# Kernel tuning notes

Measured on AMD Instinct MI355X. Metric: run time of the kernel, lower is better.

## Reference

```python
import jax, jax.numpy as jnp
import numpy as np

IMG_H, IMG_W = 800, 1216
NUM_CLASSES = 91
NUM_ANCHORS = 9
C_FPN = 256
LEVEL_HW = [(100, 152), (50, 76), (25, 38), (13, 19), (7, 10)]
SCORE_T = 0.05
NMS_T = 0.5
TOPK = 1000
MAX_DET = 300
BBOX_CLIP = float(np.log(1000.0 / 16.0))
NEG = -1e9


def make_anchors():
    # torchvision AnchorGenerator: sizes (x, x*2^(1/3), x*2^(2/3)) for x in [32..512], ratios (0.5,1,2)
    sizes = [(32, 40, 50), (64, 80, 101), (128, 161, 203), (256, 322, 406), (512, 645, 812)]
    ratios = np.array([0.5, 1.0, 2.0], dtype=np.float64)
    levels = []
    for (H, W), sc in zip(LEVEL_HW, sizes):
        scales = np.array(sc, dtype=np.float64)
        h_r = np.sqrt(ratios)
        w_r = 1.0 / h_r
        ws = (w_r[:, None] * scales[None, :]).reshape(-1)
        hs = (h_r[:, None] * scales[None, :]).reshape(-1)
        base = np.round(np.stack([-ws, -hs, ws, hs], axis=1) / 2.0)  # [9,4]
        sx = IMG_W // W
        sy = IMG_H // H
        shift_x = np.arange(W, dtype=np.float64) * sx
        shift_y = np.arange(H, dtype=np.float64) * sy
        yy, xx = np.meshgrid(shift_y, shift_x, indexing='ij')
        shifts = np.stack([xx, yy, xx, yy], axis=-1).reshape(-1, 1, 4)  # [HW,1,4]
        levels.append((shifts + base[None]).reshape(-1, 4).astype(np.float32))  # [HW*9,4]
    return levels


def _conv(x, w, b):
    y = jax.lax.conv_general_dilated(x, w, (1, 1), 'SAME', dimension_numbers=('NCHW', 'OIHW', 'NCHW'))
    return y + b[None, :, None, None]


def _gn(x, g, b, groups=32, eps=1e-5):
    N, C, H, W = x.shape
    xr = x.reshape(N, groups, C // groups, H, W)
    mu = xr.mean((2, 3, 4), keepdims=True)
    var = xr.var((2, 3, 4), keepdims=True)
    xr = (xr - mu) * jax.lax.rsqrt(var + eps)
    return xr.reshape(N, C, H, W) * g[None, :, None, None] + b[None, :, None, None]


def _tower(x, tw, tb, gs, gb):
    for i in range(4):  # fixed 4-layer conv tower
        x = jax.nn.relu(_gn(_conv(x, tw[i], tb[i]), gs[i], gb[i]))
    return x


def _decode(rel, anc):
    # torchvision BoxCoder decode, weights (1,1,1,1)
    w = anc[:, 2] - anc[:, 0]
    h = anc[:, 3] - anc[:, 1]
    cx = anc[:, 0] + 0.5 * w
    cy = anc[:, 1] + 0.5 * h
    dx, dy = rel[:, 0], rel[:, 1]
    dw = jnp.minimum(rel[:, 2], BBOX_CLIP)
    dh = jnp.minimum(rel[:, 3], BBOX_CLIP)
    pcx = dx * w + cx
    pcy = dy * h + cy
    pw = jnp.exp(dw) * w
    ph = jnp.exp(dh) * h
    return jnp.stack([pcx - 0.5 * pw, pcy - 0.5 * ph, pcx + 0.5 * pw, pcy + 0.5 * ph], axis=-1)


def _iou_one(box, boxes):
    lt = jnp.maximum(box[:2], boxes[:, :2])
    rb = jnp.minimum(box[2:], boxes[:, 2:])
    wh = jnp.clip(rb - lt, 0.0)
    inter = wh[:, 0] * wh[:, 1]
    a1 = (box[2] - box[0]) * (box[3] - box[1])
    a2 = (boxes[:, 2] - boxes[:, 0]) * (boxes[:, 3] - boxes[:, 1])
    return inter / (a1 + a2 - inter + 1e-9)


def _nms(boxes, scores, labels):
    # class-aware NMS via per-class coordinate offset, fixed MAX_DET iterations
    off = labels.astype(boxes.dtype) * float(IMG_W + IMG_H + 1)
    b_off = boxes + off[:, None]

    def body(ws, _):
        j = jnp.argmax(ws)
        s = ws[j]
        sup = _iou_one(b_off[j], b_off) > NMS_T
        ws = jnp.where(sup, NEG, ws)
        ws = ws.at[j].set(NEG)
        return ws, (j, s)

    _, (idxs, svals) = jax.lax.scan(body, scores, None, length=MAX_DET)
    valid = svals > 0.0
    out_boxes = jnp.where(valid[:, None], boxes[idxs], 0.0)
    out_scores = jnp.where(valid, svals, 0.0)
    out_labels = jnp.where(valid, labels[idxs], -1)
    return out_boxes, out_scores, out_labels


def _post_one(cls_l, reg_l, anc_l):
    bxs, scs, lbs = [], [], []
    for cl, rg, an in zip(cls_l, reg_l, anc_l):
        s = jax.nn.sigmoid(cl).reshape(-1)  # [HW*9*91]
        s = jnp.where(s > SCORE_T, s, -1.0)
        v, i = jax.lax.top_k(s, TOPK)
        ai = i // NUM_CLASSES
        lb = i % NUM_CLASSES
        bxs.append(_decode(rg[ai], an[ai]))
        scs.append(v)
        lbs.append(lb)
    boxes = jnp.concatenate(bxs)
    scores = jnp.concatenate(scs)
    labels = jnp.concatenate(lbs).astype(jnp.int32)
    boxes = jnp.stack([jnp.clip(boxes[:, 0], 0, IMG_W), jnp.clip(boxes[:, 1], 0, IMG_H),
                       jnp.clip(boxes[:, 2], 0, IMG_W), jnp.clip(boxes[:, 3], 0, IMG_H)], axis=-1)
    scores = jnp.where(scores > SCORE_T, scores, NEG)
    return _nms(boxes, scores, labels)


def setup_inputs() -> dict:
    key = jax.random.key(0)
    ks = jax.random.split(key, 16)
    d = {}
    for n, (name, (H, W)) in enumerate(zip(['p3', 'p4', 'p5', 'p6', 'p7'], LEVEL_HW)):
        d[name] = jax.random.normal(ks[n], (2, C_FPN, H, W), jnp.float32)
    std = 0.01
    d['cls_tw'] = jax.random.normal(ks[5], (4, C_FPN, C_FPN, 3, 3), jnp.float32) * std
    d['cls_tb'] = jnp.zeros((4, C_FPN), jnp.float32)
    d['cls_gs'] = jnp.ones((4, C_FPN), jnp.float32)
    d['cls_gb'] = jnp.zeros((4, C_FPN), jnp.float32)
    d['cls_w'] = jax.random.normal(ks[6], (NUM_ANCHORS * NUM_CLASSES, C_FPN, 3, 3), jnp.float32) * std
    d['cls_b'] = jnp.full((NUM_ANCHORS * NUM_CLASSES,), -float(np.log((1 - 0.01) / 0.01)), jnp.float32)
    d['reg_tw'] = jax.random.normal(ks[7], (4, C_FPN, C_FPN, 3, 3), jnp.float32) * std
    d['reg_tb'] = jnp.zeros((4, C_FPN), jnp.float32)
    d['reg_gs'] = jnp.ones((4, C_FPN), jnp.float32)
    d['reg_gb'] = jnp.zeros((4, C_FPN), jnp.float32)
    d['reg_w'] = jax.random.normal(ks[8], (NUM_ANCHORS * 4, C_FPN, 3, 3), jnp.float32) * std
    d['reg_b'] = jnp.zeros((NUM_ANCHORS * 4,), jnp.float32)
    d['anchors'] = jnp.asarray(np.concatenate(make_anchors(), axis=0))  # [A_total,4]
    return d


def reference(p3, p4, p5, p6, p7, cls_tw, cls_tb, cls_gs, cls_gb, cls_w, cls_b,
              reg_tw, reg_tb, reg_gs, reg_gb, reg_w, reg_b, anchors):
    feats = [p3, p4, p5, p6, p7]
    cls_levels, reg_levels = [], []
    for f in feats:
        N, _, H, W = f.shape
        c = _conv(_tower(f, cls_tw, cls_tb, cls_gs, cls_gb), cls_w, cls_b)
        c = c.reshape(N, NUM_ANCHORS, NUM_CLASSES, H, W).transpose(0, 3, 4, 1, 2).reshape(N, -1, NUM_CLASSES)
        cls_levels.append(c)
        r = _conv(_tower(f, reg_tw, reg_tb, reg_gs, reg_gb), reg_w, reg_b)
        r = r.reshape(N, NUM_ANCHORS, 4, H, W).transpose(0, 3, 4, 1, 2).reshape(N, -1, 4)
        reg_levels.append(r)
    sizes = [H * W * NUM_ANCHORS for (H, W) in LEVEL_HW]
    splits = np.cumsum(sizes)[:-1].tolist()
    anc_levels = tuple(jnp.split(anchors, splits, axis=0))
    boxes, scores, labels = jax.vmap(_post_one, in_axes=(0, 0, None))(
        tuple(cls_levels), tuple(reg_levels), anc_levels)
    return boxes, scores, labels
```

## Files before the change

### kernel.cpp

```cpp
#include <hip/hip_runtime.h>
#include <hip/hip_fp16.h>
#include <math.h>

#define CAP 4096
#define P_TOT 20267
#define PAD_N 21267

typedef unsigned short ushort_t;
typedef __attribute__((ext_vector_type(8))) _Float16 f16x8;
typedef __attribute__((ext_vector_type(8))) short s16x8;
typedef __attribute__((ext_vector_type(4))) float f32x4;

struct LvlSrc { const float* p[5]; };
struct Cand { float score; int level; int ai; int lb; float b0,b1,b2,b3; };
struct ConvArgs {
    const ushort_t* Ah[2]; const ushort_t* Al[2];
    ushort_t* Oh[2]; ushort_t* Ol[2];
    const float* bias[2];
    int brow0[2];
};
struct PadPtrs { ushort_t* p[8]; };

__constant__ int d_H[5]    = {100,50,25,13,7};
__constant__ int d_W[5]    = {152,76,38,19,10};
__constant__ int d_WP[5]   = {154,78,40,21,12};
__constant__ int d_HP[5]   = {102,52,27,15,9};
__constant__ int d_HW[5]   = {15200,3800,950,247,70};
__constant__ int d_LOFF[6] = {0,15200,19000,19950,20197,20267};
__constant__ int d_POFF[6] = {0,15708,19764,20844,21159,21267};
__constant__ int d_PT[6]   = {0,119,149,157,159,160};
__constant__ int d_RC[6]   = {0,508,764,894,962,1000};

__device__ __forceinline__ ushort_t f2h(float x) { return __half_as_ushort(__float2half(x)); }
__device__ __forceinline__ float h2f(ushort_t u) { return __half2float(__ushort_as_half(u)); }

__global__ void zero_pad_k(PadPtrs bufs)
{
    int idx = blockIdx.x*256 + threadIdx.x;
    if (idx >= 64000) return;
    int cs = idx & 31;
    int rest = idx >> 5;
    int n = rest & 1;
    int r = rest >> 1;
    int l = 0; while (l < 4 && r >= d_RC[l+1]) ++l;
    r -= d_RC[l];
    int WP = d_WP[l], HP = d_HP[l];
    int y, x;
    if (r < WP)            { y = 0;      x = r; }
    else if (r < 2*WP)     { y = HP-1;   x = r - WP; }
    else { int s = r - 2*WP; y = 1 + (s >> 1); x = (s & 1) ? WP-1 : 0; }
    size_t a = ((size_t)(n*PAD_N + d_POFF[l] + y*WP + x))*256 + cs*8;
    s16x8 z = (s16x8){0,0,0,0,0,0,0,0};
#pragma unroll
    for (int i = 0; i < 8; ++i) *(s16x8*)(bufs.p[i] + a) = z;
}

__global__ void sentinel_k(float* out, int nsz)
{
    int i = blockIdx.x*256 + threadIdx.x;
    if (i < nsz) out[i] = 12345.0f;
}

__global__ void prepw_k(const float* __restrict__ cls_tw, const float* __restrict__ reg_tw,
                        const float* __restrict__ cls_w, ushort_t* __restrict__ bh)
{
    size_t total = (size_t)2944*2304;
    for (size_t idx = (size_t)blockIdx.x*256 + threadIdx.x; idx < total; idx += (size_t)gridDim.x*256) {
        int k = (int)(idx % 2304); int row = (int)(idx / 2304);
        int tap = k >> 8; int ci = k & 255;
        float v;
        if (row < 1024)        v = cls_tw[(size_t)row*2304 + ci*9 + tap];
        else if (row < 2048)   v = reg_tw[(size_t)(row-1024)*2304 + ci*9 + tap];
        else { int co = row - 2048; v = (co < 819) ? cls_w[(size_t)co*2304 + ci*9 + tap] : 0.f; }
        bh[idx] = f2h(v);
    }
}

__global__ __launch_bounds__(256)
void conv_in_k(LvlSrc src, ushort_t* __restrict__ ph, ushort_t* __restrict__ pl)
{
    int total = 2*32*P_TOT;
    for (int idx = blockIdx.x*256 + threadIdx.x; idx < total; idx += gridDim.x*256) {
        int pix = idx % P_TOT;
        int cs  = (idx / P_TOT) & 31;
        int n   = idx / (32*P_TOT);
        int l = 0; while (l < 4 && pix >= d_LOFF[l+1]) ++l;
        int p = pix - d_LOFF[l];
        int W = d_W[l], WP = d_WP[l], HW = d_HW[l];
        int y = p / W, x = p % W;
        const float* sp = src.p[l];
        size_t a = ((size_t)(n*PAD_N + d_POFF[l] + (y+1)*WP + (x+1)))*256 + cs*8;
        s16x8 vh, vl;
#pragma unroll
        for (int j = 0; j < 8; ++j) {
            float v = sp[((size_t)(n*256 + cs*8 + j))*HW + p];
            ushort_t h = f2h(v);
            vh[j] = (short)h;
            vl[j] = (short)f2h(v - h2f(h));
        }
        *(s16x8*)(ph + a) = vh;
        *(s16x8*)(pl + a) = vl;
    }
}

__global__ __launch_bounds__(256)
void convmfma_k(ConvArgs args, const ushort_t* __restrict__ Bh,
                float* __restrict__ partials, int q, int detect,
                const float* __restrict__ fbias, Cand* cand, int* ccnt)
{
    __shared__ __align__(16) ushort_t smem[3*8192];
    ushort_t* sAh = smem;
    ushort_t* sAl = smem + 8192;
    ushort_t* sBh = smem + 16384;

    int b = blockIdx.x;
    int widx = (b & 7)*q + (b >> 3);
    int pt, t2, n, cot, tw, brow;
    if (!detect) {
        pt = widx >> 3; t2 = widx & 7;
        n = t2 & 1; cot = (t2 >> 1) & 1; tw = t2 >> 2; brow = args.brow0[tw] + cot*128;
    } else {
        pt = widx / 14; t2 = widx - pt*14;
        n = t2 & 1; cot = t2 >> 1; tw = 0; brow = 2048 + cot*128;
    }

    int l = 0; while (l < 4 && pt >= d_PT[l+1]) ++l;
    int p0 = (pt - d_PT[l])*128;
    int Pl = d_HW[l], W = d_W[l], WP = d_WP[l];
    const ushort_t* Ah = args.Ah[tw];
    const ushort_t* Al = args.Al[tw];

    int tid = threadIdx.x;
    int w = tid >> 6, ln = tid & 63;
    int wr = w >> 1, wc = w & 1;

    size_t abase[4]; size_t bbase[4]; int ldso[4];
#pragma unroll
    for (int it = 0; it < 4; ++it) {
        int ch = (it*4 + w)*8 + (ln >> 3);
        int swz = ((ln & 7) ^ (ch & 7)) << 3;
        int p = min(p0 + ch, Pl - 1);
        int y = p / W, x = p % W;
        abase[it] = ((size_t)(n*PAD_N + d_POFF[l] + y*WP + x))*256 + swz;
        bbase[it] = ((size_t)(brow + ch))*2304 + swz;
        ldso[it]  = (it*4 + w)*1024;
    }

    int kbase = (ln >> 4) * 8;
    int rowA[4], xrA[4], rowB[4], xrB[4];
#pragma unroll
    for (int m = 0; m < 4; ++m) {
        int r = wr*64 + m*16 + (ln & 15);
        rowA[m] = r*64; xrA[m] = (r & 7) << 3;
    }
#pragma unroll
    for (int nf = 0; nf < 4; ++nf) {
        int r = wc*64 + nf*16 + (ln & 15);
        rowB[nf] = r*64; xrB[nf] = (r & 7) << 3;
    }

    f32x4 acc[4][4];
#pragma unroll
    for (int m = 0; m < 4; ++m)
#pragma unroll
        for (int nf = 0; nf < 4; ++nf) acc[m][nf] = (f32x4){0.f,0.f,0.f,0.f};

    auto stage = [&](int ks) {
        int ky = ks / 12;
        int rem = ks - ky*12;
        int sl = rem / 3;
        int kx = rem - sl*3;
        size_t adelta = (size_t)(ky*WP + kx)*256 + sl*64;
        size_t bdelta = (size_t)((ky*3 + kx)*256 + sl*64);
#pragma unroll
        for (int it = 0; it < 4; ++it) {
            __builtin_amdgcn_global_load_lds((const unsigned int*)(Ah + abase[it] + adelta),
                                             (unsigned int*)((char*)sAh + ldso[it]), 16, 0, 0);
            __builtin_amdgcn_global_load_lds((const unsigned int*)(Al + abase[it] + adelta),
                                             (unsigned int*)((char*)sAl + ldso[it]), 16, 0, 0);
            __builtin_amdgcn_global_load_lds((const unsigned int*)(Bh + bbase[it] + bdelta),
                                             (unsigned int*)((char*)sBh + ldso[it]), 16, 0, 0);
        }
    };

    stage(0);
    for (int ks = 0; ks < 36; ++ks) {
        __syncthreads();
        f16x8 a_h[2][4], a_l[2][4], b_h[2][4];
#pragma unroll
        for (int ks2 = 0; ks2 < 2; ++ks2) {
            int kb = kbase + ks2*32;
#pragma unroll
            for (int m = 0; m < 4; ++m) {
                int idx = rowA[m] + (kb ^ xrA[m]);
                a_h[ks2][m] = *(const f16x8*)&sAh[idx];
                a_l[ks2][m] = *(const f16x8*)&sAl[idx];
            }
#pragma unroll
            for (int nf = 0; nf < 4; ++nf) {
                int idx = rowB[nf] + (kb ^ xrB[nf]);
                b_h[ks2][nf] = *(const f16x8*)&sBh[idx];
            }
        }
        __syncthreads();
        if (ks + 1 < 36) stage(ks + 1);
        __builtin_amdgcn_sched_barrier(0);
#pragma unroll
        for (int ks2 = 0; ks2 < 2; ++ks2)
#pragma unroll
            for (int m = 0; m < 4; ++m)
#pragma unroll
                for (int nf = 0; nf < 4; ++nf) {
                    acc[m][nf] = __builtin_amdgcn_mfma_f32_16x16x32_f16(a_h[ks2][m], b_h[ks2][nf], acc[m][nf], 0, 0, 0);
                    acc[m][nf] = __builtin_amdgcn_mfma_f32_16x16x32_f16(a_l[ks2][m], b_h[ks2][nf], acc[m][nf], 0, 0, 0);
                }
    }

    if (!detect) {
        ushort_t* Oh = args.Oh[tw];
        ushort_t* Ol = args.Ol[tw];
        const float* bias = args.bias[tw];
        float S[4] = {0,0,0,0}, Q[4] = {0,0,0,0};
#pragma unroll
        for (int m = 0; m < 4; ++m) {
            size_t pa[4]; bool ok[4];
#pragma unroll
            for (int r = 0; r < 4; ++r) {
                int p_row = p0 + wr*64 + m*16 + (ln >> 4)*4 + r;
                ok[r] = p_row < Pl;
                int pr = ok[r] ? p_row : 0;
                int y = pr / W, x = pr - y*W;
                pa[r] = ((size_t)(n*PAD_N + d_POFF[l] + (y+1)*WP + (x+1)))*256;
            }
#pragma unroll
            for (int nf = 0; nf < 4; ++nf) {
                int co = cot*128 + wc*64 + nf*16 + (ln & 15);
                float bs = bias[co];
#pragma unroll
                for (int r = 0; r < 4; ++r) if (ok[r]) {
                    float v = acc[m][nf][r] + bs;
                    ushort_t h = f2h(v);
                    Oh[pa[r] + co] = h;
                    Ol[pa[r] + co] = f2h(v - h2f(h));
                    S[nf] += v; Q[nf] += v*v;
                }
            }
        }
        __syncthreads();
        float* redS = (float*)smem;
        float* redQ = redS + 2048;
        float* colS = redQ + 2048;
        float* colQ = colS + 128;
#pragma unroll
        for (int nf = 0; nf < 4; ++nf) {
            int slot = ((wc*4 + nf)*16 + (ln & 15))*8 + wr*4 + (ln >> 4);
            redS[slot] = S[nf]; redQ[slot] = Q[nf];
        }
        __syncthreads();
        if (tid < 128) {
            float s = 0.f, qq = 0.f;
#pragma unroll
            for (int j = 0; j < 8; ++j) { s += redS[tid*8 + j]; qq += redQ[tid*8 + j]; }
            colS[tid] = s; colQ[tid] = qq;
        }
        __syncthreads();
        if (tid < 16) {
            float s = 0.f, qq = 0.f;
#pragma unroll
            for (int j = 0; j < 8; ++j) { s += colS[tid*8 + j]; qq += colQ[tid*8 + j]; }
            partials[((size_t)widx*16 + tid)*2]     = s;
            partials[((size_t)widx*16 + tid)*2 + 1] = qq;
        }
    } else {
        int pixbase = p0 + wr*64;
#pragma unroll
        for (int m = 0; m < 4; ++m)
#pragma unroll
            for (int nf = 0; nf < 4; ++nf) {
                int co = cot*128 + wc*64 + nf*16 + (ln & 15);
                if (co < 819) {
                    float bs = fbias[co];
#pragma unroll
                    for (int r = 0; r < 4; ++r) {
                        int p_row = pixbase + m*16 + (ln >> 4)*4 + r;
                        if (p_row < Pl) {
                            float logit = acc[m][nf][r] + bs;
                            if (logit > -2.95f) {
                                float score = 1.0f/(1.0f + expf(-logit));
                                if (score > 0.05f) {
                                    int idx = atomicAdd(&ccnt[n], 1);
                                    if (idx < CAP) {
                                        Cand c; c.score = score; c.level = l;
                                        c.ai = p_row*9 + co/91;
                                        c.lb = co % 91;
                                        c.b0 = c.b1 = c.b2 = c.b3 = 0.f;
                                        cand[n*CAP + idx] = c;
                                    }
                                }
                            }
                        }
                    }
                }
            }
    }
}

__global__ void gn_stats_k(const float* __restrict__ partials, float* __restrict__ stats)
{
    int t = blockIdx.x*32 + threadIdx.x;
    if (t >= 640) return;
    int g = t & 31, n = (t >> 5) & 1, l = (t >> 6) % 5, tw = t / 320;
    int cot = g >> 4, gi = g & 15;
    int t2 = tw*4 + cot*2 + n;
    double S = 0.0, Q = 0.0;
    for (int pt = d_PT[l]; pt < d_PT[l+1]; ++pt) {
        int widx = pt*8 + t2;
        S += (double)partials[((size_t)widx*16 + gi)*2];
        Q += (double)partials[((size_t)widx*16 + gi)*2 + 1];
    }
    double cnt = 8.0 * (double)d_HW[l];
    double mean = S / cnt;
    double var = Q / cnt - mean*mean;
    stats[t*2]     = (float)mean;
    stats[t*2 + 1] = (float)(1.0 / sqrt(var + 1e-5));
}

__global__ __launch_bounds__(256)
void gn_norm_k(ushort_t* hC, ushort_t* lC, ushort_t* hR, ushort_t* lR,
               const float* __restrict__ stats,
               const float* __restrict__ gC, const float* __restrict__ bC,
               const float* __restrict__ gR, const float* __restrict__ bR)
{
    int total = 4*P_TOT*32;
    for (int idx = blockIdx.x*256 + threadIdx.x; idx < total; idx += gridDim.x*256) {
        int cs = idx & 31;
        int pix = (idx >> 5) % P_TOT;
        int rest = (idx >> 5) / P_TOT;
        int n = rest & 1, tw = rest >> 1;
        int l = 0; while (l < 4 && pix >= d_LOFF[l+1]) ++l;
        const float* st = stats + (size_t)(tw*320 + l*64 + n*32 + cs)*2;
        float mean = st[0], rstd = st[1];
        const float* gamma = tw ? gR : gC;
        const float* beta  = tw ? bR : bC;
        ushort_t* H = tw ? hR : hC;
        ushort_t* L = tw ? lR : lC;
        int p = pix - d_LOFF[l];
        int W = d_W[l], WP = d_WP[l];
        int y = p / W, x = p % W;
        size_t a = ((size_t)(n*PAD_N + d_POFF[l] + (y+1)*WP + (x+1)))*256 + cs*8;
        s16x8 vh = *(s16x8*)(H + a);
        s16x8 vl = *(s16x8*)(L + a);
#pragma unroll
        for (int j = 0; j < 8; ++j) {
            float v = h2f((ushort_t)vh[j]) + h2f((ushort_t)vl[j]);
            v = (v - mean)*rstd*gamma[cs*8 + j] + beta[cs*8 + j];
            v = v > 0.f ? v : 0.f;
            ushort_t h = f2h(v);
            vh[j] = (short)h;
            vl[j] = (short)f2h(v - h2f(h));
        }
        *(s16x8*)(H + a) = vh;
        *(s16x8*)(L + a) = vl;
    }
}

__global__ void cand_reg_k(Cand* cand, const int* __restrict__ ccnt,
                           const ushort_t* __restrict__ fh, const ushort_t* __restrict__ fl,
                           const float* __restrict__ rw, const float* __restrict__ rb,
                           const float* __restrict__ anchors)
{
    int n = blockIdx.y;
    int id = blockIdx.x;
    int cnt = min(ccnt[n], CAP);
    if (id >= cnt) return;
    Cand c = cand[n*CAP + id];
    int l = c.level; int W = d_W[l], WP = d_WP[l];
    int pix = c.ai / 9, a = c.ai % 9;
    int y = pix / W, x = pix % W;
    int tid = threadIdx.x;
    float r0 = 0, r1 = 0, r2 = 0, r3 = 0;
    for (int k = tid; k < 2304; k += 64) {
        int ci = k / 9, tap = k % 9;
        size_t ad = ((size_t)(n*PAD_N + d_POFF[l] + (y + tap/3)*WP + (x + tap%3)))*256 + ci;
        float f = h2f(fh[ad]) + h2f(fl[ad]);
        r0 += f * rw[(a*4 + 0)*2304 + k];
        r1 += f * rw[(a*4 + 1)*2304 + k];
        r2 += f * rw[(a*4 + 2)*2304 + k];
        r3 += f * rw[(a*4 + 3)*2304 + k];
    }
    for (int off = 32; off; off >>= 1) {
        r0 += __shfl_down(r0, off);
        r1 += __shfl_down(r1, off);
        r2 += __shfl_down(r2, off);
        r3 += __shfl_down(r3, off);
    }
    if (tid == 0) {
        r0 += rb[a*4+0]; r1 += rb[a*4+1]; r2 += rb[a*4+2]; r3 += rb[a*4+3];
        const float* an = anchors + ((size_t)(d_LOFF[l]*9 + c.ai))*4;
        float aw = an[2]-an[0], ah = an[3]-an[1];
        float cx = an[0]+0.5f*aw, cy = an[1]+0.5f*ah;
        const float CLIP = 4.135166556742356f;
        float dw = fminf(r2, CLIP), dh = fminf(r3, CLIP);
        float pcx = r0*aw + cx, pcy = r1*ah + cy;
        float pw = expf(dw)*aw, ph2 = expf(dh)*ah;
        float b0 = pcx - 0.5f*pw, b1 = pcy - 0.5f*ph2;
        float b2 = pcx + 0.5f*pw, b3 = pcy + 0.5f*ph2;
        cand[n*CAP+id].b0 = fminf(fmaxf(b0, 0.f), 1216.f);
        cand[n*CAP+id].b1 = fminf(fmaxf(b1, 0.f), 800.f);
        cand[n*CAP+id].b2 = fminf(fmaxf(b2, 0.f), 1216.f);
        cand[n*CAP+id].b3 = fminf(fmaxf(b3, 0.f), 800.f);
    }
}

__global__ __launch_bounds__(256)
void nms_k(const Cand* __restrict__ cand, const int* __restrict__ ccnt, float* __restrict__ out)
{
    int n = blockIdx.x;
    int tid = threadIdx.x;
    int cnt = min(ccnt[n], CAP);
    const Cand* cd = cand + n*CAP;
    __shared__ unsigned char alive[CAP];
    __shared__ unsigned long long rK[256];
    __shared__ int rI[256];
    __shared__ float selB[4];
    float* outB = out + n*1200;
    float* outS = out + 2400 + n*300;
    float* outL = out + 3000 + n*300;
    for (int i = tid; i < 1200; i += 256) outB[i] = 0.f;
    for (int i = tid; i < 300; i += 256) { outS[i] = 0.f; outL[i] = -1.f; }
    for (int i = tid; i < CAP; i += 256) alive[i] = (i < cnt) ? 1 : 0;
    __syncthreads();
    for (int t = 0; t < 300; ++t) {
        unsigned long long bk = 0ull; int bi = -1;
        for (int i = tid; i < cnt; i += 256) if (alive[i]) {
            unsigned flat = (unsigned)(cd[i].ai*91 + cd[i].lb);
            unsigned long long k = ((unsigned long long)__float_as_uint(cd[i].score) << 32)
                                 | (unsigned long long)(0x07FFFFFFu - (((unsigned)cd[i].level << 24) | flat));
            if (k > bk) { bk = k; bi = i; }
        }
        rK[tid] = bk; rI[tid] = bi;
        __syncthreads();
        for (int off = 128; off; off >>= 1) {
            if (tid < off && rK[tid+off] > rK[tid]) { rK[tid] = rK[tid+off]; rI[tid] = rI[tid+off]; }
            __syncthreads();
        }
        if (rK[0] == 0ull) break;
        if (tid == 0) {
            int j = rI[0];
            Cand s = cd[j];
            alive[j] = 0;
            outB[t*4+0] = s.b0; outB[t*4+1] = s.b1; outB[t*4+2] = s.b2; outB[t*4+3] = s.b3;
            outS[t] = s.score; outL[t] = (float)s.lb;
            float o = (float)s.lb * 2017.0f;
            selB[0] = s.b0+o; selB[1] = s.b1+o; selB[2] = s.b2+o; selB[3] = s.b3+o;
        }
        __syncthreads();
        float s0 = selB[0], s1 = selB[1], s2 = selB[2], s3 = selB[3];
        float a1 = (s2-s0)*(s3-s1);
        for (int i = tid; i < cnt; i += 256) if (alive[i]) {
            float o = (float)cd[i].lb * 2017.0f;
            float c0 = cd[i].b0+o, c1 = cd[i].b1+o, c2 = cd[i].b2+o, c3 = cd[i].b3+o;
            float ltx = fmaxf(s0,c0), lty = fmaxf(s1,c1);
            float rbx = fminf(s2,c2), rby = fminf(s3,c3);
            float w = fmaxf(rbx-ltx, 0.f), h = fmaxf(rby-lty, 0.f);
            float inter = w*h;
            float a2 = (c2-c0)*(c3-c1);
            float iou = inter/(a1 + a2 - inter + 1e-9f);
            if (iou > 0.5f) alive[i] = 0;
        }
        __syncthreads();
    }
}

extern "C" void kernel_launch(void* const* d_in, const int* in_sizes, int n_in,
                              void* d_out, int out_size, void* d_ws, size_t ws_size,
                              hipStream_t stream)
{
    const float* p[5];
    for (int i = 0; i < 5; ++i) p[i] = (const float*)d_in[i];
    const float* cls_tw = (const float*)d_in[5];
    const float* cls_tb = (const float*)d_in[6];
    const float* cls_gs = (const float*)d_in[7];
    const float* cls_gb = (const float*)d_in[8];
    const float* cls_w  = (const float*)d_in[9];
    const float* cls_b  = (const float*)d_in[10];
    const float* reg_tw = (const float*)d_in[11];
    const float* reg_tb = (const float*)d_in[12];
    const float* reg_gs = (const float*)d_in[13];
    const float* reg_gb = (const float*)d_in[14];
    const float* reg_w  = (const float*)d_in[15];
    const float* reg_b  = (const float*)d_in[16];
    const float* anchors= (const float*)d_in[17];

    size_t PADB = (size_t)2*PAD_N*256;
    char* ws = (char*)d_ws;
    ushort_t* P0h  = (ushort_t*)ws;
    ushort_t* P0l  = P0h  + PADB;
    ushort_t* CAh  = P0l  + PADB;
    ushort_t* CAl  = CAh  + PADB;
    ushort_t* RAh  = CAl  + PADB;
    ushort_t* RAl  = RAh  + PADB;
    ushort_t* RBh  = RAl  + PADB;
    ushort_t* RBl  = RBh  + PADB;
    ushort_t* wtbH = RBl  + PADB;
    float*    partials = (float*)(wtbH + (size_t)2944*2304);
    float*    stats    = partials + (size_t)1280*16*2;
    Cand*     cand     = (Cand*)(stats + 640*2);
    int*      ccnt     = (int*)(cand + 2*CAP);
    size_t need = (size_t)((char*)(ccnt + 2) - ws);
    if (ws_size < need) {
        sentinel_k<<<(out_size + 255)/256, 256, 0, stream>>>((float*)d_out, out_size);
        return;
    }

    PadPtrs zp; zp.p[0]=P0h; zp.p[1]=P0l; zp.p[2]=CAh; zp.p[3]=CAl;
               zp.p[4]=RAh; zp.p[5]=RAl; zp.p[6]=RBh; zp.p[7]=RBl;
    zero_pad_k<<<250,256,0,stream>>>(zp);
    hipMemsetAsync(ccnt, 0, 2*sizeof(int), stream);
    prepw_k<<<4096,256,0,stream>>>(cls_tw, reg_tw, cls_w, wtbH);

    LvlSrc sIn;
    for (int l = 0; l < 5; ++l) sIn.p[l] = p[l];
    conv_in_k<<<2048,256,0,stream>>>(sIn, P0h, P0l);

    const ushort_t* sH[2]; const ushort_t* sL[2]; ushort_t* dH[2]; ushort_t* dL[2];
    for (int i = 0; i < 4; ++i) {
        if (i == 0)      { sH[0]=P0h; sL[0]=P0l; sH[1]=P0h; sL[1]=P0l; dH[0]=CAh; dL[0]=CAl; dH[1]=RAh; dL[1]=RAl; }
        else if (i == 1) { sH[0]=CAh; sL[0]=CAl; sH[1]=RAh; sL[1]=RAl; dH[0]=P0h; dL[0]=P0l; dH[1]=RBh; dL[1]=RBl; }
        else if (i == 2) { sH[0]=P0h; sL[0]=P0l; sH[1]=RBh; sL[1]=RBl; dH[0]=CAh; dL[0]=CAl; dH[1]=RAh; dL[1]=RAl; }
        else             { sH[0]=CAh; sL[0]=CAl; sH[1]=RAh; sL[1]=RAl; dH[0]=P0h; dL[0]=P0l; dH[1]=RBh; dL[1]=RBl; }
        ConvArgs a;
        a.Ah[0]=sH[0]; a.Al[0]=sL[0]; a.Ah[1]=sH[1]; a.Al[1]=sL[1];
        a.Oh[0]=dH[0]; a.Ol[0]=dL[0]; a.Oh[1]=dH[1]; a.Ol[1]=dL[1];
        a.bias[0]=cls_tb + i*256; a.bias[1]=reg_tb + i*256;
        a.brow0[0]=i*256; a.brow0[1]=1024 + i*256;
        convmfma_k<<<1280,256,0,stream>>>(a, wtbH, partials, 160, 0, nullptr, nullptr, nullptr);
        gn_stats_k<<<20,32,0,stream>>>(partials, stats);
        gn_norm_k<<<4096,256,0,stream>>>(dH[0], dL[0], dH[1], dL[1], stats,
                                         cls_gs + i*256, cls_gb + i*256,
                                         reg_gs + i*256, reg_gb + i*256);
    }

    {
        ConvArgs a;
        a.Ah[0]=P0h; a.Al[0]=P0l; a.Ah[1]=P0h; a.Al[1]=P0l;
        a.Oh[0]=nullptr; a.Ol[0]=nullptr; a.Oh[1]=nullptr; a.Ol[1]=nullptr;
        a.bias[0]=nullptr; a.bias[1]=nullptr;
        a.brow0[0]=2048; a.brow0[1]=2048;
        convmfma_k<<<2240,256,0,stream>>>(a, wtbH, nullptr, 280, 1, cls_b, cand, ccnt);
    }

    cand_reg_k<<<dim3(CAP,2),64,0,stream>>>(cand, ccnt, RBh, RBl, reg_w, reg_b, anchors);
    nms_k<<<2,256,0,stream>>>(cand, ccnt, (float*)d_out);
}
```

Measured before the change: 1.338 ms.

## Screen class logits with low-precision conv, refine candidates exactly

The classification-head conv is templated so the detect path uses only the high fp16 half of the activations. That halves its MFMA count and A-tile loads and shrinks LDS. Pixels passing a looser logit threshold are stored as packed candidate words. A new refine kernel then recomputes each candidate's logit in fp32 from the split activations before applying the score threshold. The risks are candidate overflow past CAP if the looser threshold admits too many, and a missed candidate if the fp16 error exceeds the margin.

```diff
diff --git a/kernel.cpp b/kernel.cpp
--- a/kernel.cpp
+++ b/kernel.cpp
@@ -103,20 +103,21 @@
     }
 }
 
+template<bool DETECT>
 __global__ __launch_bounds__(256)
 void convmfma_k(ConvArgs args, const ushort_t* __restrict__ Bh,
-                float* __restrict__ partials, int q, int detect,
+                float* __restrict__ partials, int q,
                 const float* __restrict__ fbias, Cand* cand, int* ccnt)
 {
-    __shared__ __align__(16) ushort_t smem[3*8192];
+    __shared__ __align__(16) ushort_t smem[(DETECT ? 2 : 3)*8192];
     ushort_t* sAh = smem;
     ushort_t* sAl = smem + 8192;
-    ushort_t* sBh = smem + 16384;
+    ushort_t* sBh = smem + (DETECT ? 8192 : 16384);
 
     int b = blockIdx.x;
     int widx = (b & 7)*q + (b >> 3);
     int pt, t2, n, cot, tw, brow;
-    if (!detect) {
+    if (!DETECT) {
         pt = widx >> 3; t2 = widx & 7;
         n = t2 & 1; cot = (t2 >> 1) & 1; tw = t2 >> 2; brow = args.brow0[tw] + cot*128;
     } else {
@@ -176,8 +177,9 @@
         for (int it = 0; it < 4; ++it) {
             __builtin_amdgcn_global_load_lds((const unsigned int*)(Ah + abase[it] + adelta),
                                              (unsigned int*)((char*)sAh + ldso[it]), 16, 0, 0);
-            __builtin_amdgcn_global_load_lds((const unsigned int*)(Al + abase[it] + adelta),
-                                             (unsigned int*)((char*)sAl + ldso[it]), 16, 0, 0);
+            if constexpr (!DETECT)
+                __builtin_amdgcn_global_load_lds((const unsigned int*)(Al + abase[it] + adelta),
+                                                 (unsigned int*)((char*)sAl + ldso[it]), 16, 0, 0);
             __builtin_amdgcn_global_load_lds((const unsigned int*)(Bh + bbase[it] + bdelta),
                                              (unsigned int*)((char*)sBh + ldso[it]), 16, 0, 0);
         }
@@ -194,7 +196,7 @@
             for (int m = 0; m < 4; ++m) {
                 int idx = rowA[m] + (kb ^ xrA[m]);
                 a_h[ks2][m] = *(const f16x8*)&sAh[idx];
-                a_l[ks2][m] = *(const f16x8*)&sAl[idx];
+                if constexpr (!DETECT) a_l[ks2][m] = *(const f16x8*)&sAl[idx];
             }
 #pragma unroll
             for (int nf = 0; nf < 4; ++nf) {
@@ -212,11 +214,12 @@
 #pragma unroll
                 for (int nf = 0; nf < 4; ++nf) {
                     acc[m][nf] = __builtin_amdgcn_mfma_f32_16x16x32_f16(a_h[ks2][m], b_h[ks2][nf], acc[m][nf], 0, 0, 0);
-                    acc[m][nf] = __builtin_amdgcn_mfma_f32_16x16x32_f16(a_l[ks2][m], b_h[ks2][nf], acc[m][nf], 0, 0, 0);
+                    if constexpr (!DETECT)
+                        acc[m][nf] = __builtin_amdgcn_mfma_f32_16x16x32_f16(a_l[ks2][m], b_h[ks2][nf], acc[m][nf], 0, 0, 0);
                 }
     }
 
-    if (!detect) {
+    if constexpr (!DETECT) {
         ushort_t* Oh = args.Oh[tw];
         ushort_t* Ol = args.Ol[tw];
         const float* bias = args.bias[tw];
@@ -272,6 +275,7 @@
             partials[((size_t)widx*16 + tid)*2 + 1] = qq;
         }
     } else {
+        unsigned* pcand = (unsigned*)cand;
         int pixbase = p0 + wr*64;
 #pragma unroll
         for (int m = 0; m < 4; ++m)
@@ -285,23 +289,54 @@
                         int p_row = pixbase + m*16 + (ln >> 4)*4 + r;
                         if (p_row < Pl) {
                             float logit = acc[m][nf][r] + bs;
-                            if (logit > -2.95f) {
-                                float score = 1.0f/(1.0f + expf(-logit));
-                                if (score > 0.05f) {
-                                    int idx = atomicAdd(&ccnt[n], 1);
-                                    if (idx < CAP) {
-                                        Cand c; c.score = score; c.level = l;
-                                        c.ai = p_row*9 + co/91;
-                                        c.lb = co % 91;
-                                        c.b0 = c.b1 = c.b2 = c.b3 = 0.f;
-                                        cand[n*CAP + idx] = c;
-                                    }
-                                }
+                            if (logit > -3.2f) {
+                                int idx = atomicAdd(&ccnt[n], 1);
+                                if (idx < CAP)
+                                    pcand[n*CAP + idx] = ((unsigned)l << 24) | ((unsigned)co << 14) | (unsigned)p_row;
                             }
                         }
                     }
                 }
             }
+    }
+}
+
+__global__ void refine_k(const unsigned* __restrict__ pcand, const int* __restrict__ pccnt,
+                         Cand* cand, int* ccnt,
+                         const ushort_t* __restrict__ fh, const ushort_t* __restrict__ fl,
+                         const float* __restrict__ cls_w, const float* __restrict__ cls_b)
+{
+    int n = blockIdx.y;
+    int id = blockIdx.x;
+    if (id >= min(pccnt[n], CAP)) return;
+    unsigned pc = pcand[n*CAP + id];
+    int l  = pc >> 24;
+    int co = (pc >> 14) & 0x3FF;
+    int pr = pc & 0x3FFF;
+    int W = d_W[l], WP = d_WP[l];
+    int y = pr / W, x = pr % W;
+    int tid = threadIdx.x;
+    float acc = 0.f;
+    for (int k = tid; k < 2304; k += 64) {
+        int ci = k / 9, tap = k % 9;
+        size_t ad = ((size_t)(n*PAD_N + d_POFF[l] + (y + tap/3)*WP + (x + tap%3)))*256 + ci;
+        float f = h2f(fh[ad]) + h2f(fl[ad]);
+        acc += f * cls_w[(size_t)co*2304 + ci*9 + tap];
+    }
+    for (int off = 32; off; off >>= 1) acc += __shfl_down(acc, off);
+    if (tid == 0) {
+        float logit = acc + cls_b[co];
+        float score = 1.0f/(1.0f + expf(-logit));
+        if (score > 0.05f) {
+            int idx = atomicAdd(&ccnt[n], 1);
+            if (idx < CAP) {
+                Cand c; c.score = score; c.level = l;
+                c.ai = pr*9 + co/91;
+                c.lb = co % 91;
+                c.b0 = c.b1 = c.b2 = c.b3 = 0.f;
+                cand[n*CAP + idx] = c;
+            }
+        }
     }
 }
 
@@ -506,17 +541,19 @@
     float*    partials = (float*)(wtbH + (size_t)2944*2304);
     float*    stats    = partials + (size_t)1280*16*2;
     Cand*     cand     = (Cand*)(stats + 640*2);
-    int*      ccnt     = (int*)(cand + 2*CAP);
-    size_t need = (size_t)((char*)(ccnt + 2) - ws);
+    unsigned* pcand    = (unsigned*)(cand + 2*CAP);
+    int*      ccnt     = (int*)(pcand + 2*CAP);
+    size_t need = (size_t)((char*)(ccnt + 4) - ws);
     if (ws_size < need) {
         sentinel_k<<<(out_size + 255)/256, 256, 0, stream>>>((float*)d_out, out_size);
         return;
     }
+    int* pccnt = ccnt + 2;
 
     PadPtrs zp; zp.p[0]=P0h; zp.p[1]=P0l; zp.p[2]=CAh; zp.p[3]=CAl;
                zp.p[4]=RAh; zp.p[5]=RAl; zp.p[6]=RBh; zp.p[7]=RBl;
     zero_pad_k<<<250,256,0,stream>>>(zp);
-    hipMemsetAsync(ccnt, 0, 2*sizeof(int), stream);
+    hipMemsetAsync(ccnt, 0, 4*sizeof(int), stream);
     prepw_k<<<4096,256,0,stream>>>(cls_tw, reg_tw, cls_w, wtbH);
 
     LvlSrc sIn;
@@ -534,7 +571,7 @@
         a.Oh[0]=dH[0]; a.Ol[0]=dL[0]; a.Oh[1]=dH[1]; a.Ol[1]=dL[1];
         a.bias[0]=cls_tb + i*256; a.bias[1]=reg_tb + i*256;
         a.brow0[0]=i*256; a.brow0[1]=1024 + i*256;
-        convmfma_k<<<1280,256,0,stream>>>(a, wtbH, partials, 160, 0, nullptr, nullptr, nullptr);
+        convmfma_k<false><<<1280,256,0,stream>>>(a, wtbH, partials, 160, nullptr, nullptr, nullptr);
         gn_stats_k<<<20,32,0,stream>>>(partials, stats);
         gn_norm_k<<<4096,256,0,stream>>>(dH[0], dL[0], dH[1], dL[1], stats,
                                          cls_gs + i*256, cls_gb + i*256,
@@ -547,8 +584,9 @@
         a.Oh[0]=nullptr; a.Ol[0]=nullptr; a.Oh[1]=nullptr; a.Ol[1]=nullptr;
         a.bias[0]=nullptr; a.bias[1]=nullptr;
         a.brow0[0]=2048; a.brow0[1]=2048;
-        convmfma_k<<<2240,256,0,stream>>>(a, wtbH, nullptr, 280, 1, cls_b, cand, ccnt);
-    }
+        convmfma_k<true><<<2240,256,0,stream>>>(a, wtbH, nullptr, 280, cls_b, (Cand*)pcand, pccnt);
+    }
+    refine_k<<<dim3(CAP,2),64,0,stream>>>(pcand, pccnt, cand, ccnt, P0h, P0l, cls_w, cls_b);
 
     cand_reg_k<<<dim3(CAP,2),64,0,stream>>>(cand, ccnt, RBh, RBl, reg_w, reg_b, anchors);
     nms_k<<<2,256,0,stream>>>(cand, ccnt, (float*)d_out);
```

Result: faster. 1.260 ms, median of 2 (-5.9%).
